# Kernel tuning notes

Measured on AMD Instinct MI355X. Metric: run time of the kernel, lower is better.

Reference implementation:

```python
import jax, jax.numpy as jnp
import numpy as np

D_MODEL = 2048
N_HEADS = 16
HEAD_DIM = D_MODEL // N_HEADS  # 128
SCALE_BASE = 512


def rotate_half(x):
    x1, x2 = jnp.split(x, 2, axis=-1)
    return jnp.concatenate((-x2, x1), axis=-1)


def rotary_xpos(seq_len, dim, dtype=jnp.float32):
    inv_freq = 1.0 / (10000.0 ** (jnp.arange(0, dim, 2, dtype=jnp.float32) / dim))
    t = jnp.arange(seq_len, dtype=jnp.float32)
    freqs = jnp.einsum('i,j->ij', t, inv_freq)
    freqs = jnp.concatenate((freqs, freqs), axis=-1)  # [S, dim]
    scale_base = (jnp.arange(0, dim, 2, dtype=jnp.float32) + 0.4 * dim) / (1.4 * dim)
    power = (t - seq_len // 2) / SCALE_BASE
    scale = scale_base[None, :] ** power[:, None]  # [S, dim/2]
    scale = jnp.concatenate((scale, scale), axis=-1)  # [S, dim]
    return freqs.astype(dtype), scale.astype(dtype)


def apply_rotary(t, pos, scale):
    return t * jnp.cos(pos) * scale + rotate_half(t) * jnp.sin(pos) * scale


def setup_inputs() -> dict:
    key = jax.random.key(0)
    ks = jax.random.split(key, 5)
    B, S = 2, 2048
    hidden_states = jax.random.normal(ks[0], (B, S, D_MODEL), dtype=jnp.float32)
    # Linear weights stored as [out, in] like torch; we use x @ W.T
    w_q = jax.random.normal(ks[1], (N_HEADS * HEAD_DIM, D_MODEL), dtype=jnp.float32) * 0.02
    w_kv = jax.random.normal(ks[2], (2 * HEAD_DIM, D_MODEL), dtype=jnp.float32) * 0.02
    w_proj = jax.random.normal(ks[3], (D_MODEL, N_HEADS * HEAD_DIM), dtype=jnp.float32) * 0.02
    b_proj = jax.random.normal(ks[4], (D_MODEL,), dtype=jnp.float32) * 0.02
    return {"hidden_states": hidden_states, "w_q": w_q, "w_kv": w_kv,
            "w_proj": w_proj, "b_proj": b_proj}


def reference(hidden_states, w_q, w_kv, w_proj, b_proj):
    B, S, _ = hidden_states.shape
    q = hidden_states @ w_q.T                      # [B,S,H*D]
    kv = hidden_states @ w_kv.T                    # [B,S,2*D]
    k, v = jnp.split(kv, 2, axis=-1)               # [B,S,D] each
    q = q.reshape(B, S, N_HEADS, HEAD_DIM).transpose(0, 2, 1, 3)  # [B,H,S,D]

    scale_w = HEAD_DIM ** (-0.5)
    q = q * scale_w
    k = k * scale_w

    pos, xscale = rotary_xpos(S, HEAD_DIM, q.dtype)
    q = apply_rotary(q, pos, xscale)               # broadcast [S,D] over [B,H,S,D]
    k = apply_rotary(k, pos, 1.0 / xscale)         # [B,S,D]

    attn = jnp.einsum('bnih,bjh->bnij', q, k)      # [B,H,S,S]
    causal = jnp.triu(jnp.ones((S, S), dtype=bool), 1)
    attn = jnp.where(causal, -jnp.finfo(attn.dtype).max, attn)
    attn = jax.nn.softmax(attn, axis=-1)

    out = jnp.einsum('bnij,bjd->bind', attn, v)    # [B,S,H,D]
    out = out.reshape(B, S, N_HEADS * HEAD_DIM)
    out = out @ w_proj.T + b_proj
    return out
```

## Files before the change

### kernel.cpp

```cpp
#include <hip/hip_runtime.h>
#include <math.h>

typedef __bf16 bf16;
typedef __bf16 bf16x8 __attribute__((ext_vector_type(8)));
typedef float f32x4 __attribute__((ext_vector_type(4)));
typedef float f32x16 __attribute__((ext_vector_type(16)));

#define MFMA16(a, b, c) __builtin_amdgcn_mfma_f32_16x16x32_bf16((a), (b), (c), 0, 0, 0)
#define MFMA32(a, b, c) __builtin_amdgcn_mfma_f32_32x32x16_bf16((a), (b), (c), 0, 0, 0)

__device__ __forceinline__ float clampf(float v, float lo, float hi) {
  return fminf(fmaxf(v, lo), hi);
}

__device__ __forceinline__ void async_copy16(const void* g, void* l) {
  __builtin_amdgcn_global_load_lds(
      (__attribute__((address_space(1))) void*)g,
      (__attribute__((address_space(3))) void*)l,
      16, 0, 0);
}

__device__ __forceinline__ unsigned cvtpk(float a, float b) {
  unsigned r;
  asm("v_cvt_pk_bf16_f32 %0, %1, %2" : "=v"(r) : "v"(a), "v"(b));
  return r;
}

__device__ __forceinline__ void pl32swap(unsigned& a, unsigned& b, int hi) {
#if __has_builtin(__builtin_amdgcn_permlane32_swap)
  auto r = __builtin_amdgcn_permlane32_swap(a, b, false, false);
  a = r[0];
  b = r[1];
#else
  unsigned ax = (unsigned)__shfl_xor((int)a, 32, 64);
  unsigned bx = (unsigned)__shfl_xor((int)b, 32, 64);
  unsigned o0 = hi ? bx : a;
  unsigned o1 = hi ? b : ax;
  a = o0; b = o1;
#endif
}

__device__ __forceinline__ bf16x8 frag4(unsigned d0, unsigned d1, unsigned d2, unsigned d3) {
  union { unsigned u[4]; bf16x8 v; } t;
  t.u[0] = d0; t.u[1] = d1; t.u[2] = d2; t.u[3] = d3;
  return t.v;
}


__global__ void convert_bf16(const float* __restrict__ hs,
                             const float* __restrict__ wq,
                             const float* __restrict__ wkv,
                             const float* __restrict__ wproj,
                             bf16* __restrict__ hs_bf,
                             bf16* __restrict__ wqkv_bf,
                             bf16* __restrict__ wproj_bf) {
  const long long v = (long long)blockIdx.x * blockDim.x + threadIdx.x;
  const float* src;
  bf16* dst;
  long long off;
  if (v < 1048576) { src = hs; dst = hs_bf; off = v; }
  else if (v < 1572864) { src = wq; dst = wqkv_bf; off = v - 1048576; }
  else if (v < 1638400) { src = wkv; dst = wqkv_bf + 4194304; off = v - 1572864; }
  else { src = wproj; dst = wproj_bf; off = v - 1638400; }
  const f32x4* p = (const f32x4*)(src + off * 8);
  f32x4 f0 = p[0], f1 = p[1];
  bf16x8 r;
#pragma unroll
  for (int i = 0; i < 4; ++i) { r[i] = (bf16)f0[i]; r[i + 4] = (bf16)f1[i]; }
  *(bf16x8*)(dst + off * 8) = r;
}

__global__ __launch_bounds__(256, 2)
void gemm_qkv(const bf16* __restrict__ A, const bf16* __restrict__ Bw,
              bf16* __restrict__ Cq, bf16* __restrict__ Ckv) {
  const int K = 2048;
  __shared__ bf16 As[128 * 32];
  __shared__ bf16 Bs[128 * 32];
  const int tid = threadIdx.x;
  const int wave = tid >> 6, lane = tid & 63;
  const int quad = lane >> 4, l15 = lane & 15;
  const int r4 = lane >> 2, c4 = lane & 3;
  const int wm = wave >> 1, wn = wave & 1;
  const int orig = blockIdx.x + 18 * blockIdx.y;
  const int wgid = (orig & 7) * 72 + (orig >> 3);
  const int bx = wgid % 18;
  const int bm = (wgid / 18) * 128;
  const bf16* Bp = Bw + (size_t)bx * 128 * K;

  const f32x4 vzero = {0.f, 0.f, 0.f, 0.f};
  f32x4 acc[4][4];
#pragma unroll
  for (int i = 0; i < 4; ++i)
#pragma unroll
    for (int j = 0; j < 4; ++j) acc[i][j] = vzero;

  for (int kt = 0; kt < K; kt += 32) {
    __syncthreads();
#pragma unroll
    for (int q = 0; q < 2; ++q) {
      const int chunk = wave * 2 + q;
      const int row = chunk * 16 + r4;
      async_copy16(A + (size_t)(bm + row) * K + kt + c4 * 8, (char*)As + chunk * 1024);
      async_copy16(Bp + (size_t)row * K + kt + c4 * 8, (char*)Bs + chunk * 1024);
    }
    __syncthreads();
    bf16x8 af[4], bfr[4];
#pragma unroll
    for (int i = 0; i < 4; ++i)
      af[i] = *(const bf16x8*)((const char*)As + (wm * 64 + i * 16 + l15) * 64 + quad * 16);
#pragma unroll
    for (int i = 0; i < 4; ++i)
      bfr[i] = *(const bf16x8*)((const char*)Bs + (wn * 64 + i * 16 + l15) * 64 + quad * 16);
#pragma unroll
    for (int mi = 0; mi < 4; ++mi)
#pragma unroll
      for (int ni = 0; ni < 4; ++ni)
        acc[mi][ni] = MFMA16(af[mi], bfr[ni], acc[mi][ni]);
  }

  bf16* Cp;
  int ldc, cn;
  if (bx < 16) { Cp = Cq; ldc = 2048; cn = bx * 128; }
  else { Cp = Ckv; ldc = 256; cn = (bx - 16) * 128; }
#pragma unroll
  for (int mi = 0; mi < 4; ++mi)
#pragma unroll
    for (int ni = 0; ni < 4; ++ni) {
      const int col = cn + wn * 64 + ni * 16 + l15;
#pragma unroll
      for (int r = 0; r < 4; ++r) {
        const int row = bm + wm * 64 + mi * 16 + quad * 4 + r;
        Cp[(size_t)row * ldc + col] = (bf16)clampf(acc[mi][ni][r], -1000.f, 1000.f);
      }
    }
}

__global__ __launch_bounds__(256, 2)
void gemm_proj(const bf16* __restrict__ A, const bf16* __restrict__ Bw,
               const float* __restrict__ bias, float* __restrict__ C) {
  const int K = 2048;
  __shared__ bf16 As[128 * 32];
  __shared__ bf16 Bs[128 * 32];
  const int tid = threadIdx.x;
  const int wave = tid >> 6, lane = tid & 63;
  const int quad = lane >> 4, l15 = lane & 15;
  const int r4 = lane >> 2, c4 = lane & 3;
  const int wm = wave >> 1, wn = wave & 1;
  const int orig = blockIdx.x + 16 * blockIdx.y;
  const int wgid = (orig & 7) * 64 + (orig >> 3);
  const int bn = (wgid % 16) * 128;
  const int bm = (wgid / 16) * 128;
  const bf16* Bp = Bw + (size_t)bn * K;

  const f32x4 vzero = {0.f, 0.f, 0.f, 0.f};
  f32x4 acc[4][4];
#pragma unroll
  for (int i = 0; i < 4; ++i)
#pragma unroll
    for (int j = 0; j < 4; ++j) acc[i][j] = vzero;

  for (int kt = 0; kt < K; kt += 32) {
    __syncthreads();
#pragma unroll
    for (int q = 0; q < 2; ++q) {
      const int chunk = wave * 2 + q;
      const int row = chunk * 16 + r4;
      async_copy16(A + (size_t)(bm + row) * K + kt + c4 * 8, (char*)As + chunk * 1024);
      async_copy16(Bp + (size_t)row * K + kt + c4 * 8, (char*)Bs + chunk * 1024);
    }
    __syncthreads();
    bf16x8 af[4], bfr[4];
#pragma unroll
    for (int i = 0; i < 4; ++i)
      af[i] = *(const bf16x8*)((const char*)As + (wm * 64 + i * 16 + l15) * 64 + quad * 16);
#pragma unroll
    for (int i = 0; i < 4; ++i)
      bfr[i] = *(const bf16x8*)((const char*)Bs + (wn * 64 + i * 16 + l15) * 64 + quad * 16);
#pragma unroll
    for (int mi = 0; mi < 4; ++mi)
#pragma unroll
      for (int ni = 0; ni < 4; ++ni)
        acc[mi][ni] = MFMA16(af[mi], bfr[ni], acc[mi][ni]);
  }

#pragma unroll
  for (int mi = 0; mi < 4; ++mi)
#pragma unroll
    for (int ni = 0; ni < 4; ++ni) {
      const int col = bn + wn * 64 + ni * 16 + l15;
      const float bv = bias[col];
#pragma unroll
      for (int r = 0; r < 4; ++r) {
        const int row = bm + wm * 64 + mi * 16 + quad * 4 + r;
        C[(size_t)row * 2048 + col] = clampf(acc[mi][ni][r] + bv, -1000.f, 1000.f);
      }
    }
}

__global__ void rotary_kernel(bf16* __restrict__ Cq, bf16* __restrict__ Ckv,
                              bf16* __restrict__ VT) {
  const int row = blockIdx.x;
  const int b = row >> 11, s = row & 2047;
  const int t = threadIdx.x;
  const float power = (float)(s - 1024) * (1.0f / 512.0f);
  const float scale_w = 0.08838834764831845f;
  const float k_if = 0.2076205059304679f;

  const int h = t >> 4;
  const int j0 = (t & 15) * 4;
  const size_t qbase = (size_t)row * 2048 + (size_t)h * 128;
#pragma unroll
  for (int u = 0; u < 4; ++u) {
    const int j = j0 + u;
    const float pos = (float)s * exp2f(-k_if * (float)j);
    const float c = cosf(pos), sn = sinf(pos);
    const float sb = ((float)(2 * j) + 51.2f) * (1.0f / 179.2f);
    const float xs = exp2f(power * log2f(sb));
    const float f = xs * scale_w;
    const float q1 = (float)Cq[qbase + j];
    const float q2 = (float)Cq[qbase + j + 64];
    Cq[qbase + j]      = (bf16)((q1 * c - q2 * sn) * f);
    Cq[qbase + j + 64] = (bf16)((q2 * c + q1 * sn) * f);
  }

  if (t < 64) {
    const int j = t;
    const float pos = (float)s * exp2f(-k_if * (float)j);
    const float c = cosf(pos), sn = sinf(pos);
    const float sb = ((float)(2 * j) + 51.2f) * (1.0f / 179.2f);
    const float xs = exp2f(power * log2f(sb));
    const float f = scale_w / xs;
    const size_t kvb = (size_t)row * 256;
    const float k1 = (float)Ckv[kvb + j];
    const float k2 = (float)Ckv[kvb + j + 64];
    Ckv[kvb + j]      = (bf16)((k1 * c - k2 * sn) * f);
    Ckv[kvb + j + 64] = (bf16)((k2 * c + k1 * sn) * f);
  } else if (t < 128) {
    const int d = (t - 64) * 2;
    const size_t kvb = (size_t)row * 256 + 128;
    VT[((size_t)b * 128 + d) * 2048 + s]     = Ckv[kvb + d];
    VT[((size_t)b * 128 + d + 1) * 2048 + s] = Ckv[kvb + d + 1];
  }
}

__global__ __launch_bounds__(256, 2)
void flash_attn(const bf16* __restrict__ Qp, const bf16* __restrict__ Kkv,
                const bf16* __restrict__ VT, bf16* __restrict__ O) {
  __shared__ bf16 Ks[2][64 * 128];
  __shared__ bf16 Vs[2][128 * 64];

  const int tid = threadIdx.x;
  const int wave = tid >> 6, lane = tid & 63;
  const int hi = lane >> 5, l31 = lane & 31, l15 = lane & 15, l7 = lane & 7;
  const int bh = blockIdx.x, b = bh >> 4, h = bh & 15;
  const int L = blockIdx.y;
  const int y = (L < 8) ? L : 23 - L;
  const int nkv = 2 * y + 2;
  const int q0 = y * 128;
  const int wrow = wave * 32;

  const bf16* Kb = Kkv + (size_t)b * 2048 * 256;
  const bf16* Vb = VT + (size_t)b * 128 * 2048;

  f32x16 sacc[2];
  f32x16 oacc[4];
  bf16x8 qb[8];
  float lacc = 0.f;
  const f32x16 vz16 = {0.f, 0.f, 0.f, 0.f, 0.f, 0.f, 0.f, 0.f,
                       0.f, 0.f, 0.f, 0.f, 0.f, 0.f, 0.f, 0.f};
#pragma unroll
  for (int nt = 0; nt < 4; ++nt) oacc[nt] = vz16;

#pragma unroll
  for (int ks = 0; ks < 8; ++ks)
    qb[ks] = *(const bf16x8*)(Qp + ((size_t)(b * 2048 + q0 + wrow + l31)) * 2048 +
                              h * 128 + ks * 16 + hi * 8);

  auto stage = [&](int kv0, int buf) {
#pragma unroll
    for (int t = 0; t < 4; ++t) {
      const int ii = wave * 4 + t;
      const int kvr = ii * 4 + (lane >> 4);
      async_copy16(Kb + (size_t)(kv0 + kvr) * 256 + 8 * ((lane & 15) ^ (kvr & 15)),
                   (char*)Ks[buf] + ii * 1024);
    }
#pragma unroll
    for (int t = 0; t < 4; ++t) {
      const int jj = wave * 4 + t;
      const int dr = jj * 8 + (lane >> 3);
      async_copy16(Vb + (size_t)dr * 2048 + kv0 + 8 * ((lane & 7) ^ (dr & 7)),
                   (char*)Vs[buf] + jj * 1024);
    }
  };

  stage(0, 0);

  for (int jt = 0; jt < nkv; ++jt) {
    const int kv0 = jt * 64;
    const int buf = jt & 1;
    __syncthreads();
    if (jt + 1 < nkv) stage(kv0 + 64, buf ^ 1);

    if (kv0 <= q0 + wrow + 31) {
      sacc[0] = vz16;
      sacc[1] = vz16;
      __builtin_amdgcn_s_setprio(1);
#pragma unroll
      for (int ks = 0; ks < 8; ++ks) {
        const int sl = ((2 * ks + hi) ^ l15) << 4;
        bf16x8 ka0 = *(const bf16x8*)((const char*)Ks[buf] + l31 * 256 + sl);
        bf16x8 ka1 = *(const bf16x8*)((const char*)Ks[buf] + (32 + l31) * 256 + sl);
        sacc[0] = MFMA32(ka0, qb[ks], sacc[0]);
        sacc[1] = MFMA32(ka1, qb[ks], sacc[1]);
      }
      __builtin_amdgcn_s_setprio(0);

      const int qg = q0 + wrow + l31;
      float p[32];
      if (kv0 + 63 > q0 + wrow) {
#pragma unroll
        for (int mt = 0; mt < 2; ++mt)
#pragma unroll
          for (int r = 0; r < 16; ++r) {
            const int kg = kv0 + mt * 32 + (r & 3) + 8 * (r >> 2) + 4 * hi;
            p[mt * 16 + r] = (kg > qg) ? 0.0f : __expf(sacc[mt][r]);
          }
      } else {
#pragma unroll
        for (int mt = 0; mt < 2; ++mt)
#pragma unroll
          for (int r = 0; r < 16; ++r)
            p[mt * 16 + r] = __expf(sacc[mt][r]);
      }
#pragma unroll
      for (int i = 0; i < 32; ++i) lacc += p[i];

      bf16x8 pa[4];
#pragma unroll
      for (int mt = 0; mt < 2; ++mt) {
        const int o = mt * 16;
        unsigned a0 = cvtpk(p[o + 0], p[o + 1]);
        unsigned b0 = cvtpk(p[o + 4], p[o + 5]);
        pl32swap(a0, b0, hi);
        unsigned a1 = cvtpk(p[o + 2], p[o + 3]);
        unsigned b1 = cvtpk(p[o + 6], p[o + 7]);
        pl32swap(a1, b1, hi);
        pa[mt * 2 + 0] = frag4(a0, a1, b0, b1);
        unsigned a2 = cvtpk(p[o + 8], p[o + 9]);
        unsigned b2 = cvtpk(p[o + 12], p[o + 13]);
        pl32swap(a2, b2, hi);
        unsigned a3 = cvtpk(p[o + 10], p[o + 11]);
        unsigned b3 = cvtpk(p[o + 14], p[o + 15]);
        pl32swap(a3, b3, hi);
        pa[mt * 2 + 1] = frag4(a2, a3, b2, b3);
      }

      __builtin_amdgcn_s_setprio(1);
#pragma unroll
      for (int ks = 0; ks < 4; ++ks) {
        const int sl = ((2 * ks + hi) ^ l7) << 4;
#pragma unroll
        for (int nt = 0; nt < 4; ++nt) {
          bf16x8 vb = *(const bf16x8*)((const char*)Vs[buf] + (nt * 32 + l31) * 128 + sl);
          oacc[nt] = MFMA32(pa[ks], vb, oacc[nt]);
        }
      }
      __builtin_amdgcn_s_setprio(0);
    }
  }

  {
    const float lt = lacc + __shfl_xor(lacc, 32, 64);
    const float linv = 1.0f / lt;
    float li[16];
#pragma unroll
    for (int r = 0; r < 16; ++r)
      li[r] = __shfl(linv, (r & 3) + 8 * (r >> 2) + 4 * hi, 64);
#pragma unroll
    for (int nt = 0; nt < 4; ++nt)
#pragma unroll
      for (int r = 0; r < 16; ++r) {
        const int qr = (r & 3) + 8 * (r >> 2) + 4 * hi;
        const int s = q0 + wrow + qr;
        O[((size_t)(b * 2048 + s)) * 2048 + h * 128 + nt * 32 + l31] =
            (bf16)(oacc[nt][r] * li[r]);
      }
  }
}

extern "C" void kernel_launch(void* const* d_in, const int* in_sizes, int n_in,
                              void* d_out, int out_size, void* d_ws, size_t ws_size,
                              hipStream_t stream) {
  const float* hs     = (const float*)d_in[0];
  const float* w_q    = (const float*)d_in[1];
  const float* w_kv   = (const float*)d_in[2];
  const float* w_proj = (const float*)d_in[3];
  const float* b_proj = (const float*)d_in[4];
  float* out = (float*)d_out;
  bf16* Qbuf  = (bf16*)d_out;
  bf16* hs_bf = (bf16*)((char*)d_out + 16777216);

  char* ws = (char*)d_ws;
  bf16* Ckv      = (bf16*)(ws);
  bf16* VT       = (bf16*)(ws + 2097152);
  bf16* AO       = (bf16*)(ws + 3145728);
  bf16* wqkv_bf  = (bf16*)(ws + 19922944);
  bf16* wproj_bf = (bf16*)(ws + 29360128);

  convert_bf16<<<dim3(8448), dim3(256), 0, stream>>>(hs, w_q, w_kv, w_proj,
                                                     hs_bf, wqkv_bf, wproj_bf);
  gemm_qkv<<<dim3(18, 32), dim3(256), 0, stream>>>(hs_bf, wqkv_bf, Qbuf, Ckv);
  rotary_kernel<<<dim3(4096), dim3(256), 0, stream>>>(Qbuf, Ckv, VT);
  flash_attn<<<dim3(32, 16), dim3(256), 0, stream>>>(Qbuf, Ckv, VT, AO);
  gemm_proj<<<dim3(16, 32), dim3(256), 0, stream>>>(AO, wproj_bf, b_proj, out);
}
```

Baseline: 276.3 us.

## Split each KV tile across wave pairs in flash attention with LDS reduction

Doubles the flash attention block to 512 threads (8 waves). Each pair of waves shares 32 query rows, and each wave in the pair handles one 32-column half of the 64-wide KV tile, so per-wave work and register use are halved. At the end the partial output accumulators and row sums are reduced through LDS, reusing the K/V staging buffers. The aim is more waves in flight to hide latency, at the cost of an extra LDS reduction and barrier, plus launch bounds asking for 4 blocks per CU.

```diff
diff --git a/kernel.cpp b/kernel.cpp
--- a/kernel.cpp
+++ b/kernel.cpp
@@ -243,26 +243,28 @@
   }
 }
 
-__global__ __launch_bounds__(256, 2)
+__global__ __launch_bounds__(512, 4)
 void flash_attn(const bf16* __restrict__ Qp, const bf16* __restrict__ Kkv,
                 const bf16* __restrict__ VT, bf16* __restrict__ O) {
   __shared__ bf16 Ks[2][64 * 128];
   __shared__ bf16 Vs[2][128 * 64];
+  __shared__ float Lbuf[8 * 64];
 
   const int tid = threadIdx.x;
   const int wave = tid >> 6, lane = tid & 63;
   const int hi = lane >> 5, l31 = lane & 31, l15 = lane & 15, l7 = lane & 7;
+  const int sub = wave >> 1, mt = wave & 1;
   const int bh = blockIdx.x, b = bh >> 4, h = bh & 15;
   const int L = blockIdx.y;
   const int y = (L < 8) ? L : 23 - L;
   const int nkv = 2 * y + 2;
   const int q0 = y * 128;
-  const int wrow = wave * 32;
+  const int q0s = q0 + sub * 32;
 
   const bf16* Kb = Kkv + (size_t)b * 2048 * 256;
   const bf16* Vb = VT + (size_t)b * 128 * 2048;
 
-  f32x16 sacc[2];
+  f32x16 sacc;
   f32x16 oacc[4];
   bf16x8 qb[8];
   float lacc = 0.f;
@@ -273,20 +275,20 @@
 
 #pragma unroll
   for (int ks = 0; ks < 8; ++ks)
-    qb[ks] = *(const bf16x8*)(Qp + ((size_t)(b * 2048 + q0 + wrow + l31)) * 2048 +
+    qb[ks] = *(const bf16x8*)(Qp + ((size_t)(b * 2048 + q0s + l31)) * 2048 +
                               h * 128 + ks * 16 + hi * 8);
 
   auto stage = [&](int kv0, int buf) {
 #pragma unroll
-    for (int t = 0; t < 4; ++t) {
-      const int ii = wave * 4 + t;
+    for (int t = 0; t < 2; ++t) {
+      const int ii = wave * 2 + t;
       const int kvr = ii * 4 + (lane >> 4);
       async_copy16(Kb + (size_t)(kv0 + kvr) * 256 + 8 * ((lane & 15) ^ (kvr & 15)),
                    (char*)Ks[buf] + ii * 1024);
     }
 #pragma unroll
-    for (int t = 0; t < 4; ++t) {
-      const int jj = wave * 4 + t;
+    for (int t = 0; t < 2; ++t) {
+      const int jj = wave * 2 + t;
       const int dr = jj * 8 + (lane >> 3);
       async_copy16(Vb + (size_t)dr * 2048 + kv0 + 8 * ((lane & 7) ^ (dr & 7)),
                    (char*)Vs[buf] + jj * 1024);
@@ -301,64 +303,55 @@
     __syncthreads();
     if (jt + 1 < nkv) stage(kv0 + 64, buf ^ 1);
 
-    if (kv0 <= q0 + wrow + 31) {
-      sacc[0] = vz16;
-      sacc[1] = vz16;
+    if (kv0 + 32 * mt <= q0s + 31) {
+      sacc = vz16;
       __builtin_amdgcn_s_setprio(1);
 #pragma unroll
       for (int ks = 0; ks < 8; ++ks) {
         const int sl = ((2 * ks + hi) ^ l15) << 4;
-        bf16x8 ka0 = *(const bf16x8*)((const char*)Ks[buf] + l31 * 256 + sl);
-        bf16x8 ka1 = *(const bf16x8*)((const char*)Ks[buf] + (32 + l31) * 256 + sl);
-        sacc[0] = MFMA32(ka0, qb[ks], sacc[0]);
-        sacc[1] = MFMA32(ka1, qb[ks], sacc[1]);
+        bf16x8 ka = *(const bf16x8*)((const char*)Ks[buf] + (32 * mt + l31) * 256 + sl);
+        sacc = MFMA32(ka, qb[ks], sacc);
       }
       __builtin_amdgcn_s_setprio(0);
 
-      const int qg = q0 + wrow + l31;
-      float p[32];
-      if (kv0 + 63 > q0 + wrow) {
-#pragma unroll
-        for (int mt = 0; mt < 2; ++mt)
-#pragma unroll
-          for (int r = 0; r < 16; ++r) {
-            const int kg = kv0 + mt * 32 + (r & 3) + 8 * (r >> 2) + 4 * hi;
-            p[mt * 16 + r] = (kg > qg) ? 0.0f : __expf(sacc[mt][r]);
-          }
+      const int qg = q0s + l31;
+      float p[16];
+      if (kv0 + 32 * mt + 31 > q0s) {
+#pragma unroll
+        for (int r = 0; r < 16; ++r) {
+          const int kg = kv0 + 32 * mt + (r & 3) + 8 * (r >> 2) + 4 * hi;
+          p[r] = (kg > qg) ? 0.0f : __expf(sacc[r]);
+        }
       } else {
 #pragma unroll
-        for (int mt = 0; mt < 2; ++mt)
-#pragma unroll
-          for (int r = 0; r < 16; ++r)
-            p[mt * 16 + r] = __expf(sacc[mt][r]);
-      }
-#pragma unroll
-      for (int i = 0; i < 32; ++i) lacc += p[i];
-
-      bf16x8 pa[4];
-#pragma unroll
-      for (int mt = 0; mt < 2; ++mt) {
-        const int o = mt * 16;
-        unsigned a0 = cvtpk(p[o + 0], p[o + 1]);
-        unsigned b0 = cvtpk(p[o + 4], p[o + 5]);
+        for (int r = 0; r < 16; ++r)
+          p[r] = __expf(sacc[r]);
+      }
+#pragma unroll
+      for (int i = 0; i < 16; ++i) lacc += p[i];
+
+      bf16x8 pa[2];
+      {
+        unsigned a0 = cvtpk(p[0], p[1]);
+        unsigned b0 = cvtpk(p[4], p[5]);
         pl32swap(a0, b0, hi);
-        unsigned a1 = cvtpk(p[o + 2], p[o + 3]);
-        unsigned b1 = cvtpk(p[o + 6], p[o + 7]);
+        unsigned a1 = cvtpk(p[2], p[3]);
+        unsigned b1 = cvtpk(p[6], p[7]);
         pl32swap(a1, b1, hi);
-        pa[mt * 2 + 0] = frag4(a0, a1, b0, b1);
-        unsigned a2 = cvtpk(p[o + 8], p[o + 9]);
-        unsigned b2 = cvtpk(p[o + 12], p[o + 13]);
+        pa[0] = frag4(a0, a1, b0, b1);
+        unsigned a2 = cvtpk(p[8], p[9]);
+        unsigned b2 = cvtpk(p[12], p[13]);
         pl32swap(a2, b2, hi);
-        unsigned a3 = cvtpk(p[o + 10], p[o + 11]);
-        unsigned b3 = cvtpk(p[o + 14], p[o + 15]);
+        unsigned a3 = cvtpk(p[10], p[11]);
+        unsigned b3 = cvtpk(p[14], p[15]);
         pl32swap(a3, b3, hi);
-        pa[mt * 2 + 1] = frag4(a2, a3, b2, b3);
+        pa[1] = frag4(a2, a3, b2, b3);
       }
 
       __builtin_amdgcn_s_setprio(1);
 #pragma unroll
-      for (int ks = 0; ks < 4; ++ks) {
-        const int sl = ((2 * ks + hi) ^ l7) << 4;
+      for (int ks = 0; ks < 2; ++ks) {
+        const int sl = ((4 * mt + 2 * ks + hi) ^ l7) << 4;
 #pragma unroll
         for (int nt = 0; nt < 4; ++nt) {
           bf16x8 vb = *(const bf16x8*)((const char*)Vs[buf] + (nt * 32 + l31) * 128 + sl);
@@ -369,8 +362,29 @@
     }
   }
 
-  {
-    const float lt = lacc + __shfl_xor(lacc, 32, 64);
+  __syncthreads();
+  Lbuf[wave * 64 + lane] = lacc;
+  const int pair = sub;
+  char* mreg = (pair < 2) ? ((char*)Ks + pair * 16384)
+                          : ((char*)Vs + (pair - 2) * 16384);
+  if (mt == 1) {
+    float* dst = (float*)mreg;
+#pragma unroll
+    for (int nt = 0; nt < 4; ++nt)
+#pragma unroll
+      for (int r = 0; r < 16; ++r)
+        dst[(nt * 16 + r) * 64 + lane] = oacc[nt][r];
+  }
+  __syncthreads();
+  if (mt == 0) {
+    const float* src = (const float*)mreg;
+#pragma unroll
+    for (int nt = 0; nt < 4; ++nt)
+#pragma unroll
+      for (int r = 0; r < 16; ++r)
+        oacc[nt][r] += src[(nt * 16 + r) * 64 + lane];
+    const float lsum = lacc + Lbuf[(wave + 1) * 64 + lane];
+    const float lt = lsum + __shfl_xor(lsum, 32, 64);
     const float linv = 1.0f / lt;
     float li[16];
 #pragma unroll
@@ -381,7 +395,7 @@
 #pragma unroll
       for (int r = 0; r < 16; ++r) {
         const int qr = (r & 3) + 8 * (r >> 2) + 4 * hi;
-        const int s = q0 + wrow + qr;
+        const int s = q0s + qr;
         O[((size_t)(b * 2048 + s)) * 2048 + h * 128 + nt * 32 + l31] =
             (bf16)(oacc[nt][r] * li[r]);
       }
@@ -411,6 +425,6 @@
                                                      hs_bf, wqkv_bf, wproj_bf);
   gemm_qkv<<<dim3(18, 32), dim3(256), 0, stream>>>(hs_bf, wqkv_bf, Qbuf, Ckv);
   rotary_kernel<<<dim3(4096), dim3(256), 0, stream>>>(Qbuf, Ckv, VT);
-  flash_attn<<<dim3(32, 16), dim3(256), 0, stream>>>(Qbuf, Ckv, VT, AO);
+  flash_attn<<<dim3(32, 16), dim3(512), 0, stream>>>(Qbuf, Ckv, VT, AO);
   gemm_proj<<<dim3(16, 32), dim3(256), 0, stream>>>(AO, wproj_bf, b_proj, out);
 }
```

New measurement: 324.5 us. 17.4% more time.
